# Performance work log

Hardware: AMD Instinct MI355X
Metric: run time of the kernel (lower is better)

## Reference

```python
import jax, jax.numpy as jnp
import numpy as np

N = 2048   # nodes in the input graph
NB = 2048  # nodes in the barycenter graph
D = 128    # embedding (feature) dimension
K = 16     # number of atoms (len(size_atoms))


def cost_mat(cost_s, cost_t, p_s, p_t, tran, emb_s, emb_t):
    """Fused Gromov-Wasserstein cost matrix.

    GW structural part:  (C_s^2 p_s) 1^T + 1 (p_t^T (C_t^2)^T) - 2 C_s T C_t^T
    Fused feature part:  0.5 * squared Euclidean distance between node embeddings.
    """
    f1 = (cost_s ** 2) @ p_s                     # (N, 1)
    f2 = p_t.T @ (cost_t ** 2).T                 # (1, NB)
    cost = f1 + f2 - 2.0 * (cost_s @ tran) @ cost_t.T  # (N, NB)
    # pairwise squared Euclidean distances between embeddings
    d_emb = (jnp.sum(emb_s ** 2, axis=1, keepdims=True)
             + jnp.sum(emb_t ** 2, axis=1)[None, :]
             - 2.0 * emb_s @ emb_t.T)            # (N, NB)
    return cost + 0.5 * d_emb


def setup_inputs() -> dict:
    key = jax.random.key(0)
    k = jax.random.split(key, 6)
    graph = jax.random.uniform(k[0], (N, N), dtype=jnp.float32)
    embedding = jax.random.normal(k[1], (N, D), dtype=jnp.float32)
    prob = jnp.ones((N, 1), jnp.float32) / N           # uniform node distribution
    graph_b = jax.random.uniform(k[2], (NB, NB), dtype=jnp.float32)
    embedding_b = jax.random.normal(k[3], (NB, D), dtype=jnp.float32)
    prob_b = jnp.ones((NB, 1), jnp.float32) / NB
    t = jax.random.uniform(k[4], (N, NB), dtype=jnp.float32)
    tran = t / jnp.sum(t)                              # valid coupling-like plan (sums to 1)
    weights = jax.nn.softmax(jax.random.normal(k[5], (K,), dtype=jnp.float32))
    return {"graph": graph, "embedding": embedding, "prob": prob,
            "graph_b": graph_b, "embedding_b": embedding_b, "prob_b": prob_b,
            "tran": tran, "weights": weights, "ole_coeff": 1, "idx": 0}


def reference(graph, embedding, prob, graph_b, embedding_b, prob_b, tran, weights, ole_coeff, idx):
    # NOTE: the torch forward also computes cluster/entropy (OLE) losses from
    # `weights`, but they do NOT enter the returned value, which is only
    # <cost_mat(...), tran>. We therefore return exactly that inner product.
    cost = cost_mat(graph, graph_b, prob, prob_b, tran, embedding, embedding_b)
    return jnp.sum(cost * tran)
```

## Files before the change

### kernel.cpp

```cpp
#include <hip/hip_runtime.h>
#include <hip/hip_bf16.h>

#define NN 2048
#define DD 128

typedef unsigned short u16;
typedef unsigned int u32;
typedef __attribute__((ext_vector_type(8))) short bf16x8;
typedef __attribute__((ext_vector_type(4))) float f32x4;

__device__ __forceinline__ u16 f2bf(float f){
  u32 u = __float_as_uint(f);
  u32 r = (u + 0x7fffu + ((u >> 16) & 1u)) >> 16;
  return (u16)r;
}

__device__ __forceinline__ void gload16(const void* g, void* l){
  __builtin_amdgcn_global_load_lds(
      (const __attribute__((address_space(1))) u32*)g,
      (__attribute__((address_space(3))) u32*)l, 16, 0, 0);
}


__device__ __forceinline__ void rowpass_graph_body(
    int bid, int tid, const float* __restrict__ src, const float* __restrict__ w,
    u16* __restrict__ dst, float* __restrict__ red){
  int wid = tid >> 6, lane = tid & 63;
  int row = bid * 4 + wid;
  const float4* s4 = (const float4*)(src + (size_t)row * NN);
  float acc = 0.f;
  #pragma unroll
  for (int it = 0; it < NN / 256; ++it){
    int c4 = it * 64 + lane;
    float4 v = s4[c4];
    float4 ww = ((const float4*)w)[c4];
    acc += v.x*v.x*ww.x + v.y*v.y*ww.y + v.z*v.z*ww.z + v.w*v.w*ww.w;
    ushort4 o; o.x = f2bf(v.x); o.y = f2bf(v.y); o.z = f2bf(v.z); o.w = f2bf(v.w);
    ((ushort4*)(dst + (size_t)row * NN))[c4] = o;
  }
  #pragma unroll
  for (int off = 32; off; off >>= 1) acc += __shfl_down(acc, off);
  if (lane == 0) red[row] = acc;
}

__device__ __forceinline__ void tran_pass_body(
    int bx, int by, int t, float (*tile)[65],
    const float* __restrict__ src,
    u16* __restrict__ Tm, u16* __restrict__ Tt,
    float* __restrict__ rs, float* __restrict__ cls)
{
  int r0 = bx * 64, c0 = by * 64;
  #pragma unroll
  for (int it = 0; it < 4; ++it){
    int chunk = it * 256 + t; int r = chunk >> 4, c4 = chunk & 15;
    float4 v = ((const float4*)(src + (size_t)(r0 + r) * NN + c0))[c4];
    tile[r][c4*4+0] = v.x; tile[r][c4*4+1] = v.y;
    tile[r][c4*4+2] = v.z; tile[r][c4*4+3] = v.w;
    ushort4 o; o.x = f2bf(v.x); o.y = f2bf(v.y); o.z = f2bf(v.z); o.w = f2bf(v.w);
    ((ushort4*)(Tm + (size_t)(r0 + r) * NN + c0))[c4] = o;
  }
  __syncthreads();
  #pragma unroll
  for (int it = 0; it < 4; ++it){
    int chunk = it * 256 + t; int j = chunk >> 4, i4 = chunk & 15;
    ushort4 o;
    o.x = f2bf(tile[i4*4+0][j]); o.y = f2bf(tile[i4*4+1][j]);
    o.z = f2bf(tile[i4*4+2][j]); o.w = f2bf(tile[i4*4+3][j]);
    ((ushort4*)(Tt + (size_t)(c0 + j) * NN + r0))[i4] = o;
  }
  if (t < 64){
    float s = 0.f;
    #pragma unroll
    for (int c = 0; c < 64; ++c) s += tile[t][c];
    atomicAdd(&rs[r0 + t], s);
  } else if (t < 128){
    int c = t - 64; float s = 0.f;
    #pragma unroll
    for (int r = 0; r < 64; ++r) s += tile[r][c];
    atomicAdd(&cls[c0 + c], s);
  }
}

__device__ __forceinline__ void graphb_pass_body(
    int bx, int by, int t, float (*tile)[65], float* pb,
    const float* __restrict__ src, const float* __restrict__ probb,
    u16* __restrict__ CtT, float* __restrict__ f2)
{
  int r0 = bx * 64, c0 = by * 64;
  if (t < 64) pb[t] = probb[c0 + t];
  #pragma unroll
  for (int it = 0; it < 4; ++it){
    int chunk = it * 256 + t; int r = chunk >> 4, c4 = chunk & 15;
    float4 v = ((const float4*)(src + (size_t)(r0 + r) * NN + c0))[c4];
    tile[r][c4*4+0] = v.x; tile[r][c4*4+1] = v.y;
    tile[r][c4*4+2] = v.z; tile[r][c4*4+3] = v.w;
  }
  __syncthreads();
  #pragma unroll
  for (int it = 0; it < 4; ++it){
    int chunk = it * 256 + t; int j = chunk >> 4, i4 = chunk & 15;
    ushort4 o;
    o.x = f2bf(tile[i4*4+0][j]); o.y = f2bf(tile[i4*4+1][j]);
    o.z = f2bf(tile[i4*4+2][j]); o.w = f2bf(tile[i4*4+3][j]);
    ((ushort4*)(CtT + (size_t)(c0 + j) * NN + r0))[i4] = o;
  }
  if (t < 64){
    float s = 0.f;
    #pragma unroll
    for (int c = 0; c < 64; ++c){ float v = tile[t][c]; s += v * v * pb[c]; }
    atomicAdd(&f2[r0 + t], s);
  }
}

__device__ __forceinline__ void emb_body(
    int bid, int t, const float* __restrict__ src, u16* __restrict__ dst,
    float* __restrict__ nrm){
  int rloc = t >> 5, lane32 = t & 31;
  int row = bid * 8 + rloc;
  float4 v = ((const float4*)(src + (size_t)row * DD))[lane32];
  float a = v.x*v.x + v.y*v.y + v.z*v.z + v.w*v.w;
  ushort4 o; o.x = f2bf(v.x); o.y = f2bf(v.y); o.z = f2bf(v.z); o.w = f2bf(v.w);
  ((ushort4*)(dst + (size_t)row * DD))[lane32] = o;
  #pragma unroll
  for (int off = 16; off; off >>= 1) a += __shfl_down(a, off, 32);
  if (lane32 == 0) nrm[row] = a;
}

__global__ __launch_bounds__(256) void k_prep(
    const float* __restrict__ graph,  const float* __restrict__ prob,
    const float* __restrict__ tran,   const float* __restrict__ graphb,
    const float* __restrict__ probb,  const float* __restrict__ emb,
    const float* __restrict__ embb,
    u16* Cs, u16* Tm, u16* Tt, u16* CtT, u16* es, u16* et,
    float* f1, float* f2, float* rs, float* cls, float* ss, float* st)
{
  __shared__ float tile[64][65];
  __shared__ float pb[64];
  int b = blockIdx.x, t = threadIdx.x;
  if (b < 512){
    rowpass_graph_body(b, t, graph, prob, Cs, f1);
  } else if (b < 1536){
    int b2 = b - 512;  tran_pass_body(b2 & 31, b2 >> 5, t, tile, tran, Tm, Tt, rs, cls);
  } else if (b < 2560){
    int b2 = b - 1536; graphb_pass_body(b2 & 31, b2 >> 5, t, tile, pb, graphb, probb, CtT, f2);
  } else if (b < 2816){
    emb_body(b - 2560, t, emb, es, ss);
  } else {
    emb_body(b - 2816, t, embb, et, st);
  }
}

__global__ __launch_bounds__(512, 2) void k_gw(
    const u16* __restrict__ Cs, const u16* __restrict__ Tt,
    const u16* __restrict__ Tm, const u16* __restrict__ CtT,
    float* __restrict__ accs)
{
  __shared__ u16 lds[2][4][8192];
  const int tid = threadIdx.x;
  const int bid = blockIdx.x;
  const int swz = (bid & 7) * 32 + (bid >> 3);
  const int bi = swz >> 4, bk = swz & 15;

  const u16* srcs[4] = {Cs, Tt, Tm, CtT};
  const int panels[4] = {bi * 128, bk * 128, bi * 128, bk * 128};

  const int w = tid >> 6, lane = tid & 63;
  const int l15 = lane & 15, g = lane >> 4;
  const int gsel = w >> 2, wg = w & 3, wr = wg >> 1, wc = wg & 1;

  const int s_row = tid >> 3;
  const int s_gslot = (tid & 7) ^ (s_row & 7);

  f32x4 acc[4][4];
  #pragma unroll
  for (int m = 0; m < 4; ++m)
    #pragma unroll
    for (int n = 0; n < 4; ++n)
      acc[m][n] = (f32x4){0.f, 0.f, 0.f, 0.f};

  int offA[4][2], offB[4][2];
  #pragma unroll
  for (int m = 0; m < 4; ++m){
    int row = wr * 64 + m * 16 + l15;
    int rowb = wc * 64 + m * 16 + l15;
    #pragma unroll
    for (int kk = 0; kk < 2; ++kk){
      offA[m][kk] = row * 64 + ((((kk << 2) | g)) ^ (row & 7)) * 8;
      offB[m][kk] = rowb * 64 + ((((kk << 2) | g)) ^ (rowb & 7)) * 8;
    }
  }

  auto stage = [&](int buf, int kt){
    const size_t col = (size_t)kt * 64 + s_gslot * 8;
    #pragma unroll
    for (int tt = 0; tt < 4; ++tt){
      gload16(srcs[tt] + (size_t)(panels[tt] + s_row) * NN + col,
              &lds[buf][tt][w * 512]);
      gload16(srcs[tt] + (size_t)(panels[tt] + s_row + 64) * NN + col,
              &lds[buf][tt][4096 + w * 512]);
    }
  };

  const int NT = NN / 64;
  stage(0, 0);
  stage(1, 1);
  for (int kt = 0; kt < NT; ++kt){
    int cur = kt & 1;
    asm volatile("s_waitcnt vmcnt(8)" ::: "memory");
    __builtin_amdgcn_s_barrier();

    const u16* tA = &lds[cur][gsel * 2][0];
    const u16* tB = &lds[cur][gsel * 2 + 1][0];
    bf16x8 av[4][2], bv[4][2];
    #pragma unroll
    for (int kk = 0; kk < 2; ++kk){
      #pragma unroll
      for (int m = 0; m < 4; ++m) av[m][kk] = *(const bf16x8*)(tA + offA[m][kk]);
      #pragma unroll
      for (int n = 0; n < 4; ++n) bv[n][kk] = *(const bf16x8*)(tB + offB[n][kk]);
    }
    asm volatile("s_waitcnt lgkmcnt(0)" ::: "memory");
    __builtin_amdgcn_sched_barrier(0);
    __builtin_amdgcn_s_barrier();

    int kn = (kt + 2 < NT) ? (kt + 2) : (NT - 1);
    stage(cur, kn);

    #pragma unroll
    for (int kk = 0; kk < 2; ++kk)
      #pragma unroll
      for (int m = 0; m < 4; ++m)
        #pragma unroll
        for (int n = 0; n < 4; ++n)
          acc[m][n] = __builtin_amdgcn_mfma_f32_16x16x32_bf16(av[m][kk], bv[n][kk], acc[m][n], 0, 0, 0);
  }

  __syncthreads();

  float* ustash = (float*)&lds[0][0][0];
  if (gsel == 0){
    #pragma unroll
    for (int m = 0; m < 4; ++m)
      #pragma unroll
      for (int n = 0; n < 4; ++n)
        #pragma unroll
        for (int r = 0; r < 4; ++r){
          int row = wr * 64 + m * 16 + g * 4 + r;
          int col = wc * 64 + n * 16 + l15;
          ustash[row * 128 + col] = acc[m][n][r];
        }
  }
  __syncthreads();
  if (gsel == 1){
    float part = 0.f;
    #pragma unroll
    for (int m = 0; m < 4; ++m)
      #pragma unroll
      for (int n = 0; n < 4; ++n)
        #pragma unroll
        for (int r = 0; r < 4; ++r){
          int row = wr * 64 + m * 16 + g * 4 + r;
          int col = wc * 64 + n * 16 + l15;
          part += acc[m][n][r] * ustash[row * 128 + col];
        }
    #pragma unroll
    for (int off = 32; off; off >>= 1) part += __shfl_down(part, off);
    if (lane == 0) atomicAdd(&accs[0], part);
  }
}

__global__ __launch_bounds__(256, 2) void k_embdot(
    const u16* __restrict__ es, const u16* __restrict__ et,
    const float* __restrict__ tran, float* __restrict__ accs)
{
  __shared__ u16 lds[2][16384];
  const int tid = threadIdx.x;
  const int bid = blockIdx.x;
  const int swz = (bid & 7) * 32 + (bid >> 3);
  const int bi = swz >> 4, bj = swz & 15;
  const int w = tid >> 6, lane = tid & 63;
  const int l15 = lane & 15, g = lane >> 4;
  const int wr = w >> 1, wc = w & 1;

  const u16* srcs[2] = {es, et};
  const int panels[2] = {bi * 128, bj * 128};

  #pragma unroll
  for (int tt = 0; tt < 2; ++tt){
    #pragma unroll
    for (int it = 0; it < 8; ++it){
      int chunk = w * 8 + it;
      int r = chunk * 4 + g;
      int s = l15 ^ (r & 15);
      gload16(srcs[tt] + (size_t)(panels[tt] + r) * DD + s * 8,
              &lds[tt][chunk * 512]);
    }
  }
  __syncthreads();

  f32x4 acc[4][4];
  #pragma unroll
  for (int m = 0; m < 4; ++m)
    #pragma unroll
    for (int n = 0; n < 4; ++n)
      acc[m][n] = (f32x4){0.f, 0.f, 0.f, 0.f};

  #pragma unroll
  for (int ks = 0; ks < 4; ++ks){
    bf16x8 av[4], bv[4];
    #pragma unroll
    for (int m = 0; m < 4; ++m){
      int row = wr * 64 + m * 16 + l15;
      int sp = (ks * 4 + g) ^ (row & 15);
      av[m] = *(const bf16x8*)((const char*)&lds[0][0] + row * 256 + sp * 16);
    }
    #pragma unroll
    for (int n = 0; n < 4; ++n){
      int rowb = wc * 64 + n * 16 + l15;
      int spb = (ks * 4 + g) ^ (rowb & 15);
      bv[n] = *(const bf16x8*)((const char*)&lds[1][0] + rowb * 256 + spb * 16);
    }
    #pragma unroll
    for (int m = 0; m < 4; ++m)
      #pragma unroll
      for (int n = 0; n < 4; ++n)
        acc[m][n] = __builtin_amdgcn_mfma_f32_16x16x32_bf16(av[m], bv[n], acc[m][n], 0, 0, 0);
  }

  float part = 0.f;
  #pragma unroll
  for (int m = 0; m < 4; ++m)
    #pragma unroll
    for (int n = 0; n < 4; ++n)
      #pragma unroll
      for (int r = 0; r < 4; ++r){
        int row = bi * 128 + wr * 64 + m * 16 + g * 4 + r;
        int col = bj * 128 + wc * 64 + n * 16 + l15;
        part += tran[(size_t)row * NN + col] * acc[m][n][r];
      }
  #pragma unroll
  for (int off = 32; off; off >>= 1) part += __shfl_down(part, off);
  if (lane == 0) atomicAdd(&accs[1], part);
}

__global__ void k_final(const float* __restrict__ f1, const float* __restrict__ f2,
                        const float* __restrict__ rowsum, const float* __restrict__ colsum,
                        const float* __restrict__ ss, const float* __restrict__ st,
                        const float* __restrict__ accs, float* out){
  __shared__ float red[256];
  int t = threadIdx.x;
  float part = 0.f;
  for (int i = t; i < NN; i += 256){
    part += (f1[i] + 0.5f * ss[i]) * rowsum[i];
    part += (f2[i] + 0.5f * st[i]) * colsum[i];
  }
  red[t] = part; __syncthreads();
  for (int s = 128; s; s >>= 1){ if (t < s) red[t] += red[t + s]; __syncthreads(); }
  if (t == 0){
    float total = red[0] - 2.0f * accs[0] - accs[1];
    out[0] = total;
  }
}

extern "C" void kernel_launch(void* const* d_in, const int* in_sizes, int n_in,
                              void* d_out, int out_size, void* d_ws, size_t ws_size,
                              hipStream_t stream)
{
  const float* graph  = (const float*)d_in[0];
  const float* emb    = (const float*)d_in[1];
  const float* prob   = (const float*)d_in[2];
  const float* graphb = (const float*)d_in[3];
  const float* embb   = (const float*)d_in[4];
  const float* probb  = (const float*)d_in[5];
  const float* tran   = (const float*)d_in[6];
  (void)in_sizes; (void)n_in; (void)out_size; (void)ws_size;

  char* ws = (char*)d_ws;
  u16* Cs   = (u16*)(ws + 0);
  u16* Tm   = (u16*)(ws + 8388608);
  u16* Tt   = (u16*)(ws + 16777216);
  u16* CtT  = (u16*)(ws + 25165824);
  u16* es   = (u16*)(ws + 33554432);
  u16* et   = (u16*)(ws + 34078720);
  float* f1   = (float*)(ws + 34603008);
  float* f2   = (float*)(ws + 34611200);
  float* rs   = (float*)(ws + 34619392);
  float* cls  = (float*)(ws + 34627584);
  float* ss   = (float*)(ws + 34635776);
  float* st   = (float*)(ws + 34643968);
  float* accs = (float*)(ws + 34652160);

  hipMemsetAsync(ws + 34603008, 0, 49216, stream);

  k_prep<<<3072, 256, 0, stream>>>(graph, prob, tran, graphb, probb, emb, embb,
                                   Cs, Tm, Tt, CtT, es, et,
                                   f1, f2, rs, cls, ss, st);
  k_gw<<<256, 512, 0, stream>>>(Cs, Tt, Tm, CtT, accs);
  k_embdot<<<256, 256, 0, stream>>>(es, et, tran, accs);
  k_final<<<1, 256, 0, stream>>>(f1, f2, rs, cls, ss, st, accs, (float*)d_out);
}
```

Before: 92.61 us.

## Halve k_gw block to 256 threads with 64x128 warp tiles and split MFMA around barrier

Reduces the GW GEMM block from 8 to 4 waves, giving each wave a 64x128 output tile (4x8 MFMA accumulators), so every A fragment loaded from LDS is reused across twice as many B fragments. Staging now issues four 16-byte global-to-LDS loads per thread per matrix, with the vmcnt wait adjusted to match. The first k-half of the MFMAs is moved before the LDS barrier to overlap with the next stage issue. This raises per-thread register use (128 accumulator floats) and halves the waves per block, which can reduce latency hiding.

```diff
diff --git a/kernel.cpp b/kernel.cpp
--- a/kernel.cpp
+++ b/kernel.cpp
@@ -150,7 +150,7 @@
   }
 }
 
-__global__ __launch_bounds__(512, 2) void k_gw(
+__global__ __launch_bounds__(256, 1) void k_gw(
     const u16* __restrict__ Cs, const u16* __restrict__ Tt,
     const u16* __restrict__ Tm, const u16* __restrict__ CtT,
     float* __restrict__ accs)
@@ -166,38 +166,43 @@
 
   const int w = tid >> 6, lane = tid & 63;
   const int l15 = lane & 15, g = lane >> 4;
-  const int gsel = w >> 2, wg = w & 3, wr = wg >> 1, wc = wg & 1;
+  const int gsel = w >> 1, wr = w & 1;
 
   const int s_row = tid >> 3;
   const int s_gslot = (tid & 7) ^ (s_row & 7);
 
-  f32x4 acc[4][4];
+  f32x4 acc[4][8];
   #pragma unroll
   for (int m = 0; m < 4; ++m)
     #pragma unroll
-    for (int n = 0; n < 4; ++n)
+    for (int n = 0; n < 8; ++n)
       acc[m][n] = (f32x4){0.f, 0.f, 0.f, 0.f};
 
-  int offA[4][2], offB[4][2];
+  int offA[4][2], offB[8][2];
   #pragma unroll
   for (int m = 0; m < 4; ++m){
     int row = wr * 64 + m * 16 + l15;
-    int rowb = wc * 64 + m * 16 + l15;
-    #pragma unroll
-    for (int kk = 0; kk < 2; ++kk){
+    #pragma unroll
+    for (int kk = 0; kk < 2; ++kk)
       offA[m][kk] = row * 64 + ((((kk << 2) | g)) ^ (row & 7)) * 8;
-      offB[m][kk] = rowb * 64 + ((((kk << 2) | g)) ^ (rowb & 7)) * 8;
-    }
+  }
+  #pragma unroll
+  for (int n = 0; n < 8; ++n){
+    int rowb = n * 16 + l15;
+    #pragma unroll
+    for (int kk = 0; kk < 2; ++kk)
+      offB[n][kk] = rowb * 64 + ((((kk << 2) | g)) ^ (rowb & 7)) * 8;
   }
 
   auto stage = [&](int buf, int kt){
     const size_t col = (size_t)kt * 64 + s_gslot * 8;
     #pragma unroll
     for (int tt = 0; tt < 4; ++tt){
-      gload16(srcs[tt] + (size_t)(panels[tt] + s_row) * NN + col,
-              &lds[buf][tt][w * 512]);
-      gload16(srcs[tt] + (size_t)(panels[tt] + s_row + 64) * NN + col,
-              &lds[buf][tt][4096 + w * 512]);
+      #pragma unroll
+      for (int r = 0; r < 4; ++r){
+        gload16(srcs[tt] + (size_t)(panels[tt] + s_row + r * 32) * NN + col,
+                &lds[buf][tt][w * 512 + r * 2048]);
+      }
     }
   };
 
@@ -206,19 +211,25 @@
   stage(1, 1);
   for (int kt = 0; kt < NT; ++kt){
     int cur = kt & 1;
-    asm volatile("s_waitcnt vmcnt(8)" ::: "memory");
+    asm volatile("s_waitcnt vmcnt(16)" ::: "memory");
     __builtin_amdgcn_s_barrier();
 
     const u16* tA = &lds[cur][gsel * 2][0];
     const u16* tB = &lds[cur][gsel * 2 + 1][0];
-    bf16x8 av[4][2], bv[4][2];
+    bf16x8 av[4][2], bv[8][2];
     #pragma unroll
     for (int kk = 0; kk < 2; ++kk){
       #pragma unroll
       for (int m = 0; m < 4; ++m) av[m][kk] = *(const bf16x8*)(tA + offA[m][kk]);
       #pragma unroll
-      for (int n = 0; n < 4; ++n) bv[n][kk] = *(const bf16x8*)(tB + offB[n][kk]);
+      for (int n = 0; n < 8; ++n) bv[n][kk] = *(const bf16x8*)(tB + offB[n][kk]);
     }
+    #pragma unroll
+    for (int m = 0; m < 4; ++m)
+      #pragma unroll
+      for (int n = 0; n < 8; ++n)
+        acc[m][n] = __builtin_amdgcn_mfma_f32_16x16x32_bf16(av[m][0], bv[n][0], acc[m][n], 0, 0, 0);
+
     asm volatile("s_waitcnt lgkmcnt(0)" ::: "memory");
     __builtin_amdgcn_sched_barrier(0);
     __builtin_amdgcn_s_barrier();
@@ -227,12 +238,10 @@
     stage(cur, kn);
 
     #pragma unroll
-    for (int kk = 0; kk < 2; ++kk)
-      #pragma unroll
-      for (int m = 0; m < 4; ++m)
-        #pragma unroll
-        for (int n = 0; n < 4; ++n)
-          acc[m][n] = __builtin_amdgcn_mfma_f32_16x16x32_bf16(av[m][kk], bv[n][kk], acc[m][n], 0, 0, 0);
+    for (int m = 0; m < 4; ++m)
+      #pragma unroll
+      for (int n = 0; n < 8; ++n)
+        acc[m][n] = __builtin_amdgcn_mfma_f32_16x16x32_bf16(av[m][1], bv[n][1], acc[m][n], 0, 0, 0);
   }
 
   __syncthreads();
@@ -242,11 +251,11 @@
     #pragma unroll
     for (int m = 0; m < 4; ++m)
       #pragma unroll
-      for (int n = 0; n < 4; ++n)
+      for (int n = 0; n < 8; ++n)
         #pragma unroll
         for (int r = 0; r < 4; ++r){
           int row = wr * 64 + m * 16 + g * 4 + r;
-          int col = wc * 64 + n * 16 + l15;
+          int col = n * 16 + l15;
           ustash[row * 128 + col] = acc[m][n][r];
         }
   }
@@ -256,11 +265,11 @@
     #pragma unroll
     for (int m = 0; m < 4; ++m)
       #pragma unroll
-      for (int n = 0; n < 4; ++n)
+      for (int n = 0; n < 8; ++n)
         #pragma unroll
         for (int r = 0; r < 4; ++r){
           int row = wr * 64 + m * 16 + g * 4 + r;
-          int col = wc * 64 + n * 16 + l15;
+          int col = n * 16 + l15;
           part += acc[m][n][r] * ustash[row * 128 + col];
         }
     #pragma unroll
@@ -395,7 +404,7 @@
   k_prep<<<3072, 256, 0, stream>>>(graph, prob, tran, graphb, probb, emb, embb,
                                    Cs, Tm, Tt, CtT, es, et,
                                    f1, f2, rs, cls, ss, st);
-  k_gw<<<256, 512, 0, stream>>>(Cs, Tt, Tm, CtT, accs);
+  k_gw<<<256, 256, 0, stream>>>(Cs, Tt, Tm, CtT, accs);
   k_embdot<<<256, 256, 0, stream>>>(es, et, tran, accs);
   k_final<<<1, 256, 0, stream>>>(f1, f2, rs, cls, ss, st, accs, (float*)d_out);
 }
```

Result: slower. 104.4 us (+12.8%).
